# Kernel optimization log

Measured on AMD Instinct MI355X. Metric: run time of the kernel, lower is better.

The kernel has to match this reference:

```python
import jax, jax.numpy as jnp
import numpy as np

EMBED_DIM = 1024
N_HEADS = 16
HEAD_DIM = EMBED_DIM // N_HEADS
B, S = 2, 2048


def setup_inputs() -> dict:
    key = jax.random.key(0)
    ks = jax.random.split(key, 8)
    scale = 1.0 / np.sqrt(EMBED_DIM)
    return {
        "key": jax.random.normal(ks[0], (B, S, EMBED_DIM), jnp.float32),
        "query": jax.random.normal(ks[1], (B, S, EMBED_DIM), jnp.float32),
        "value": jax.random.normal(ks[2], (B, S, EMBED_DIM), jnp.float32),
        # nn.Linear weights stored [out_features, in_features], applied as x @ W.T
        "Wq": jax.random.normal(ks[3], (EMBED_DIM, EMBED_DIM), jnp.float32) * scale,
        "Wk": jax.random.normal(ks[4], (EMBED_DIM, EMBED_DIM), jnp.float32) * scale,
        "Wv": jax.random.normal(ks[5], (EMBED_DIM, EMBED_DIM), jnp.float32) * scale,
        "Wo": jax.random.normal(ks[6], (EMBED_DIM, EMBED_DIM), jnp.float32) * scale,
        "bo": jax.random.normal(ks[7], (EMBED_DIM,), jnp.float32) * scale,
    }


def reference(key, query, value, Wq, Wk, Wv, Wo, bo) -> jnp.ndarray:
    b = key.shape[0]
    # project and split heads: [B, S, E] -> [B, H, S, D]
    def split_heads(x):
        return x.reshape(b, -1, N_HEADS, HEAD_DIM).transpose(0, 2, 1, 3)
    q = split_heads(query @ Wq.T)
    k = split_heads(key @ Wk.T)
    v = split_heads(value @ Wv.T)
    scores = jnp.einsum("bhqd,bhkd->bhqk", q, k) / np.sqrt(HEAD_DIM)
    attn = jax.nn.softmax(scores, axis=-1)
    ctx = jnp.einsum("bhqk,bhkd->bhqd", attn, v)  # [B, H, S, D]
    ctx = ctx.transpose(0, 2, 1, 3).reshape(b, -1, EMBED_DIM)
    return ctx @ Wo.T + bo
```

## Files before the change

### kernel.cpp

```cpp
#include <hip/hip_runtime.h>

typedef unsigned short u16;
typedef __bf16 bf8 __attribute__((ext_vector_type(8)));
typedef __bf16 bf2 __attribute__((ext_vector_type(2)));
typedef float f4 __attribute__((ext_vector_type(4)));

typedef __attribute__((address_space(1))) const unsigned int gas_u32;
typedef __attribute__((address_space(3))) unsigned int las_u32;
#define ASYNC16(g, l) __builtin_amdgcn_global_load_lds((gas_u32*)(g), (las_u32*)(l), 16, 0, 0)

__device__ __forceinline__ u16 f2bf(float f) {
    union { float f; unsigned int u; } v; v.f = f;
    return (u16)((v.u + 0x7fffu + ((v.u >> 16) & 1u)) >> 16);
}

__device__ __forceinline__ unsigned pkbf(float lo, float hi) {
    union { bf2 v; unsigned u; } t;
    t.v[0] = (__bf16)lo;
    t.v[1] = (__bf16)hi;
    return t.u;
}

__device__ __forceinline__ float fexp2(float x) {
#if __has_builtin(__builtin_amdgcn_exp2f)
  return __builtin_amdgcn_exp2f(x);
#else
  return __expf(x * 0.69314718056f);
#endif
}

__global__ __launch_bounds__(256) void cvt_all(
    const float* __restrict__ k_, const float* __restrict__ q_, const float* __restrict__ v_,
    const float* __restrict__ wq, const float* __restrict__ wk, const float* __restrict__ wv,
    const float* __restrict__ wo, u16* __restrict__ ws) {
  size_t e = ((size_t)blockIdx.x * 256 + threadIdx.x) * 8;
  const float* src;
  if      (e <  4194304) src = k_ + e;
  else if (e <  8388608) src = q_ + (e - 4194304);
  else if (e < 12582912) src = v_ + (e - 8388608);
  else if (e < 13631488) src = wq + (e - 12582912);
  else if (e < 14680064) src = wk + (e - 13631488);
  else if (e < 15728640) src = wv + (e - 14680064);
  else                   src = wo + (e - 15728640);
  float4 f0 = ((const float4*)src)[0];
  float4 f1 = ((const float4*)src)[1];
  uint4 o;
  o.x = (unsigned)f2bf(f0.x) | ((unsigned)f2bf(f0.y) << 16);
  o.y = (unsigned)f2bf(f0.z) | ((unsigned)f2bf(f0.w) << 16);
  o.z = (unsigned)f2bf(f1.x) | ((unsigned)f2bf(f1.y) << 16);
  o.w = (unsigned)f2bf(f1.z) | ((unsigned)f2bf(f1.w) << 16);
  *(uint4*)(ws + e) = o;
}

template<int BM, bool FINAL>
__device__ __forceinline__ void gemm_tile(const u16* __restrict__ A, const u16* __restrict__ Bm,
                                          u16* __restrict__ Cb, float* __restrict__ Cf,
                                          const float* __restrict__ bias, float scale,
                                          int bm, int bn, int ldc) {
  __shared__ u16 As[BM*64];
  __shared__ u16 Bs[128*64];
  const int tid = threadIdx.x;
  const int wave = tid >> 6, lane = tid & 63;
  const int wm = wave >> 1, wn = wave & 1;
  const int quad = lane >> 4, l16 = lane & 15;
  const int MI = BM / 32;

  f4 acc[MI][4];
  const f4 zz = {0.f, 0.f, 0.f, 0.f};
  #pragma unroll
  for (int i = 0; i < MI; i++)
    #pragma unroll
    for (int j = 0; j < 4; j++) acc[i][j] = zz;

  const int kr = tid >> 3;
  const int cs = (tid & 7) ^ (kr & 7);
  const u16* ga = A  + (size_t)(bm*BM  + kr)*1024 + cs*8;
  const u16* gb = Bm + (size_t)(bn*128 + kr)*1024 + cs*8;
  u16* la = As + tid*8;
  u16* lb = Bs + tid*8;

  for (int kt = 0; kt < 1024; kt += 64) {
    #pragma unroll
    for (int p = 0; p < BM/32; p++) ASYNC16(ga + (size_t)(p*32)*1024 + kt, la + p*2048);
    #pragma unroll
    for (int p = 0; p < 4; p++)     ASYNC16(gb + (size_t)(p*32)*1024 + kt, lb + p*2048);
    __syncthreads();
    #pragma unroll
    for (int kk = 0; kk < 2; kk++) {
      bf8 af[MI];
      #pragma unroll
      for (int mi = 0; mi < MI; mi++)
        af[mi] = *(const bf8*)(As + (wm*(BM/2) + mi*16 + l16)*64 + (((kk*4 + quad) ^ (l16 & 7))*8));
      #pragma unroll
      for (int ni = 0; ni < 4; ni++) {
        bf8 bfr = *(const bf8*)(Bs + (wn*64 + ni*16 + l16)*64 + (((kk*4 + quad) ^ (l16 & 7))*8));
        #pragma unroll
        for (int mi = 0; mi < MI; mi++)
          acc[mi][ni] = __builtin_amdgcn_mfma_f32_16x16x32_bf16(af[mi], bfr, acc[mi][ni], 0, 0, 0);
      }
    }
    __syncthreads();
  }

  #pragma unroll
  for (int mi = 0; mi < MI; mi++)
    #pragma unroll
    for (int ni = 0; ni < 4; ni++) {
      const int col = bn*128 + wn*64 + ni*16 + l16;
      #pragma unroll
      for (int r = 0; r < 4; r++) {
        const int row = bm*BM + wm*(BM/2) + mi*16 + quad*4 + r;
        if (FINAL) Cf[(size_t)row*ldc + col] = acc[mi][ni][r] + bias[col];
        else       Cb[(size_t)row*ldc + col] = f2bf(acc[mi][ni][r] * scale);
      }
    }
}

#define QSCALE 0.180336880f

__global__ __launch_bounds__(256, 3) void gemm_qkv(
    const u16* __restrict__ xq, const u16* __restrict__ xk, const u16* __restrict__ xv,
    const u16* __restrict__ wq, const u16* __restrict__ wk, const u16* __restrict__ wv,
    u16* __restrict__ Qo, u16* __restrict__ Ko, u16* __restrict__ Vto) {
  if (blockIdx.z == 0)
    gemm_tile<128,false>(xq, wq, Qo, nullptr, nullptr, QSCALE, blockIdx.x, blockIdx.y, 1024);
  else if (blockIdx.z == 1)
    gemm_tile<128,false>(xk, wk, Ko, nullptr, nullptr, 1.0f, blockIdx.x, blockIdx.y, 1024);
  else
    gemm_tile<128,false>(wv, xv, Vto, nullptr, nullptr, 1.0f, blockIdx.y, blockIdx.x, 4096);
}

__global__ __launch_bounds__(256, 2) void gemm_out(
    const u16* __restrict__ ctx, const u16* __restrict__ wo,
    const float* __restrict__ bias, float* __restrict__ out) {
  gemm_tile<64,true>(ctx, wo, nullptr, out, bias, 1.0f, blockIdx.x, blockIdx.y, 1024);
}

__global__ __launch_bounds__(256, 4) void flash_attn(
    const u16* __restrict__ Qg, const u16* __restrict__ Kg,
    const u16* __restrict__ Vtg, u16* __restrict__ ctx) {
  __shared__ uint4 smem4[2208];
  u16* Ks = (u16*)smem4;
  u16* Vt = (u16*)smem4 + 8192;
  float* Of = (float*)smem4;
  float* Lf = (float*)smem4 + 2*64*68;

  const int tid = threadIdx.x;
  const int wave = tid >> 6, lane = tid & 63;
  const int quad = lane >> 4, l16 = lane & 15;
  const int wq = wave >> 1, wk = wave & 1;
  const int h = blockIdx.x, qt = blockIdx.y, b = blockIdx.z;

  bf8 qf[2][2];
  {
    const u16* qp = Qg + (size_t)(b*2048 + qt*64 + wq*32)*1024 + h*64;
    #pragma unroll
    for (int qs = 0; qs < 2; qs++)
      #pragma unroll
      for (int kc = 0; kc < 2; kc++)
        qf[qs][kc] = *(const bf8*)(qp + (size_t)(qs*16 + l16)*1024 + kc*32 + quad*8);
  }

  const f4 zz = {0.f, 0.f, 0.f, 0.f};
  f4 ot[4][2];
  float lrow[2] = {0.f, 0.f};
  #pragma unroll
  for (int ds = 0; ds < 4; ds++)
    #pragma unroll
    for (int qs = 0; qs < 2; qs++) ot[ds][qs] = zz;

  const int kr = tid >> 3;
  const u16* kga = Kg + (size_t)(b*2048 + kr)*1024 + h*64 + ((tid & 7) ^ (kr & 7))*8;
  const int vd = tid >> 4;
  const u16* vga = Vtg + (size_t)(h*64 + vd)*4096 + b*2048 + (((tid & 15) ^ vd))*8;
  u16* kld = Ks + tid*8;
  u16* vld = Vt + tid*8;

  const int prow0 = ((l16 >> 2) << 3) + (l16 & 3);
  const int prow1 = prow0 + 4;

  for (int kv0 = 0; kv0 < 2048; kv0 += 128) {
    __syncthreads();
    #pragma unroll
    for (int p = 0; p < 4; p++) ASYNC16(kga + (size_t)(kv0 + p*32)*1024, kld + p*2048);
    #pragma unroll
    for (int p = 0; p < 4; p++) ASYNC16(vga + (size_t)(p*16)*4096 + kv0, vld + p*2048);
    __syncthreads();

    #pragma unroll
    for (int kb = 0; kb < 2; kb++) {
      f4 st[2][2];
      #pragma unroll
      for (int f = 0; f < 2; f++)
        #pragma unroll
        for (int qs = 0; qs < 2; qs++) st[f][qs] = zz;
      __builtin_amdgcn_s_setprio(1);
      #pragma unroll
      for (int f = 0; f < 2; f++) {
        const int row = wk*64 + kb*32 + (f ? prow1 : prow0);
        #pragma unroll
        for (int kc = 0; kc < 2; kc++) {
          bf8 kf = *(const bf8*)(Ks + row*64 + (((kc*4 + quad) ^ (row & 7))*8));
          #pragma unroll
          for (int qs = 0; qs < 2; qs++)
            st[f][qs] = __builtin_amdgcn_mfma_f32_16x16x32_bf16(kf, qf[qs][kc], st[f][qs], 0, 0, 0);
        }
      }
      __builtin_amdgcn_s_setprio(0);
      bf8 pf[2];
      #pragma unroll
      for (int qs = 0; qs < 2; qs++) {
        float p0 = fexp2(st[0][qs][0]), p1 = fexp2(st[0][qs][1]);
        float p2 = fexp2(st[0][qs][2]), p3 = fexp2(st[0][qs][3]);
        float p4 = fexp2(st[1][qs][0]), p5 = fexp2(st[1][qs][1]);
        float p6 = fexp2(st[1][qs][2]), p7 = fexp2(st[1][qs][3]);
        lrow[qs] += ((p0 + p1) + (p2 + p3)) + ((p4 + p5) + (p6 + p7));
        union { uint4 u; bf8 v; } pu;
        pu.u.x = pkbf(p0, p1);
        pu.u.y = pkbf(p2, p3);
        pu.u.z = pkbf(p4, p5);
        pu.u.w = pkbf(p6, p7);
        pf[qs] = pu.v;
      }
      __builtin_amdgcn_s_setprio(1);
      #pragma unroll
      for (int ds = 0; ds < 4; ds++) {
        const int d = ds*16 + l16;
        bf8 vf = *(const bf8*)(Vt + d*128 + (((wk*8 + kb*4 + quad) ^ l16)*8));
        #pragma unroll
        for (int qs = 0; qs < 2; qs++)
          ot[ds][qs] = __builtin_amdgcn_mfma_f32_16x16x32_bf16(vf, pf[qs], ot[ds][qs], 0, 0, 0);
      }
      __builtin_amdgcn_s_setprio(0);
    }
  }

  __syncthreads();
  #pragma unroll
  for (int qs = 0; qs < 2; qs++) {
    lrow[qs] += __shfl_xor(lrow[qs], 16);
    lrow[qs] += __shfl_xor(lrow[qs], 32);
  }
  float* Ofw = Of + wk*(64*68);
  #pragma unroll
  for (int ds = 0; ds < 4; ds++)
    #pragma unroll
    for (int qs = 0; qs < 2; qs++)
      #pragma unroll
      for (int r = 0; r < 4; r++)
        Ofw[(wq*32 + qs*16 + l16)*68 + ds*16 + quad*4 + r] = ot[ds][qs][r];
  if (quad == 0) {
    Lf[wk*64 + wq*32 + l16]      = lrow[0];
    Lf[wk*64 + wq*32 + 16 + l16] = lrow[1];
  }
  __syncthreads();
  {
    const int qr = tid >> 2, dp = (tid & 3)*16;
    const float inv = 1.f / (Lf[qr] + Lf[64 + qr]);
    const float* o0 = Of + qr*68 + dp;
    const float* o1 = o0 + 64*68;
    unsigned ow[8];
    #pragma unroll
    for (int i = 0; i < 8; i++)
      ow[i] = pkbf((o0[2*i] + o1[2*i]) * inv, (o0[2*i+1] + o1[2*i+1]) * inv);
    u16* cp = ctx + (size_t)(b*2048 + qt*64 + qr)*1024 + h*64 + dp;
    *(uint4*)cp       = *(uint4*)&ow[0];
    *(uint4*)(cp + 8) = *(uint4*)&ow[4];
  }
}

extern "C" void kernel_launch(void* const* d_in, const int* in_sizes, int n_in,
                              void* d_out, int out_size, void* d_ws, size_t ws_size,
                              hipStream_t stream) {
  const float* key_  = (const float*)d_in[0];
  const float* query = (const float*)d_in[1];
  const float* value = (const float*)d_in[2];
  const float* Wq = (const float*)d_in[3];
  const float* Wk = (const float*)d_in[4];
  const float* Wv = (const float*)d_in[5];
  const float* Wo = (const float*)d_in[6];
  const float* bo = (const float*)d_in[7];
  float* out = (float*)d_out;

  u16* ws  = (u16*)d_ws;
  u16* xkb = ws;
  u16* xqb = ws + 4194304;
  u16* xvb = ws + 8388608;
  u16* Wqb = ws + 12582912;
  u16* Wkb = ws + 13631488;
  u16* Wvb = ws + 14680064;
  u16* Wob = ws + 15728640;
  u16* Qb  = ws + 16777216;
  u16* Kb  = ws + 20971520;
  u16* Vtb = ws + 25165824;
  u16* Cb  = ws + 29360128;

  cvt_all<<<8192, 256, 0, stream>>>(key_, query, value, Wq, Wk, Wv, Wo, ws);
  gemm_qkv<<<dim3(32, 8, 3), 256, 0, stream>>>(xqb, xkb, xvb, Wqb, Wkb, Wvb, Qb, Kb, Vtb);
  flash_attn<<<dim3(16, 32, 2), 256, 0, stream>>>(Qb, Kb, Vtb, Cb);
  gemm_out<<<dim3(64, 8), 256, 0, stream>>>(Cb, Wob, bo, out);
}
```

Baseline: 202.7 us.

## Double-buffer K/V tiles in flash attention with async prefetch of next block

```diff
diff --git a/kernel.cpp b/kernel.cpp
--- a/kernel.cpp
+++ b/kernel.cpp
@@ -136,12 +136,11 @@
   gemm_tile<64,true>(ctx, wo, nullptr, out, bias, 1.0f, blockIdx.x, blockIdx.y, 1024);
 }
 
-__global__ __launch_bounds__(256, 4) void flash_attn(
+__global__ __launch_bounds__(256, 2) void flash_attn(
     const u16* __restrict__ Qg, const u16* __restrict__ Kg,
     const u16* __restrict__ Vtg, u16* __restrict__ ctx) {
-  __shared__ uint4 smem4[2208];
-  u16* Ks = (u16*)smem4;
-  u16* Vt = (u16*)smem4 + 8192;
+  __shared__ uint4 smem4[4096];
+  u16* S = (u16*)smem4;
   float* Of = (float*)smem4;
   float* Lf = (float*)smem4 + 2*64*68;
 
@@ -173,19 +172,31 @@
   const u16* kga = Kg + (size_t)(b*2048 + kr)*1024 + h*64 + ((tid & 7) ^ (kr & 7))*8;
   const int vd = tid >> 4;
   const u16* vga = Vtg + (size_t)(h*64 + vd)*4096 + b*2048 + (((tid & 15) ^ vd))*8;
-  u16* kld = Ks + tid*8;
-  u16* vld = Vt + tid*8;
 
   const int prow0 = ((l16 >> 2) << 3) + (l16 & 3);
   const int prow1 = prow0 + 4;
 
-  for (int kv0 = 0; kv0 < 2048; kv0 += 128) {
-    __syncthreads();
-    #pragma unroll
-    for (int p = 0; p < 4; p++) ASYNC16(kga + (size_t)(kv0 + p*32)*1024, kld + p*2048);
-    #pragma unroll
-    for (int p = 0; p < 4; p++) ASYNC16(vga + (size_t)(p*16)*4096 + kv0, vld + p*2048);
-    __syncthreads();
+  #pragma unroll
+  for (int p = 0; p < 4; p++) ASYNC16(kga + (size_t)(p*32)*1024, S + tid*8 + p*2048);
+  #pragma unroll
+  for (int p = 0; p < 4; p++) ASYNC16(vga + (size_t)(p*16)*4096, S + 8192 + tid*8 + p*2048);
+
+  for (int t = 0; t < 16; t++) {
+    u16* Ks = S + (t & 1)*16384;
+    u16* Vt = Ks + 8192;
+    if (t < 15) {
+      u16* kd = S + ((t+1) & 1)*16384 + tid*8;
+      const int kv1 = (t+1)*128;
+      #pragma unroll
+      for (int p = 0; p < 4; p++) ASYNC16(kga + (size_t)(kv1 + p*32)*1024, kd + p*2048);
+      #pragma unroll
+      for (int p = 0; p < 4; p++) ASYNC16(vga + (size_t)(p*16)*4096 + kv1, kd + 8192 + p*2048);
+      asm volatile("s_waitcnt vmcnt(8)" ::: "memory");
+    } else {
+      asm volatile("s_waitcnt vmcnt(0)" ::: "memory");
+    }
+    __builtin_amdgcn_sched_barrier(0);
+    __builtin_amdgcn_s_barrier();
 
     #pragma unroll
     for (int kb = 0; kb < 2; kb++) {
@@ -233,6 +244,9 @@
       }
       __builtin_amdgcn_s_setprio(0);
     }
+
+    asm volatile("s_waitcnt lgkmcnt(0)" ::: "memory");
+    __builtin_amdgcn_s_barrier();
   }
 
   __syncthreads();
```

Result: slower. 211.5 us (+4.4%).

## Overlap next K/V tile async loads with current QK and PV compute

Applied to the files above, without the earlier changes.

```diff
diff --git a/kernel.cpp b/kernel.cpp
--- a/kernel.cpp
+++ b/kernel.cpp
@@ -179,14 +179,16 @@
   const int prow0 = ((l16 >> 2) << 3) + (l16 & 3);
   const int prow1 = prow0 + 4;
 
-  for (int kv0 = 0; kv0 < 2048; kv0 += 128) {
-    __syncthreads();
-    #pragma unroll
-    for (int p = 0; p < 4; p++) ASYNC16(kga + (size_t)(kv0 + p*32)*1024, kld + p*2048);
-    #pragma unroll
-    for (int p = 0; p < 4; p++) ASYNC16(vga + (size_t)(p*16)*4096 + kv0, vld + p*2048);
-    __syncthreads();
-
+  #pragma unroll
+  for (int p = 0; p < 4; p++) ASYNC16(kga + (size_t)(p*32)*1024, kld + p*2048);
+  #pragma unroll
+  for (int p = 0; p < 4; p++) ASYNC16(vga + (size_t)(p*16)*4096, vld + p*2048);
+  asm volatile("s_waitcnt vmcnt(4)" ::: "memory");
+  __builtin_amdgcn_sched_barrier(0);
+  __builtin_amdgcn_s_barrier();
+
+  for (int t = 0; t < 16; t++) {
+    bf8 pf[2][2];
     #pragma unroll
     for (int kb = 0; kb < 2; kb++) {
       f4 st[2][2];
@@ -207,7 +209,6 @@
         }
       }
       __builtin_amdgcn_s_setprio(0);
-      bf8 pf[2];
       #pragma unroll
       for (int qs = 0; qs < 2; qs++) {
         float p0 = fexp2(st[0][qs][0]), p1 = fexp2(st[0][qs][1]);
@@ -220,18 +221,39 @@
         pu.u.y = pkbf(p2, p3);
         pu.u.z = pkbf(p4, p5);
         pu.u.w = pkbf(p6, p7);
-        pf[qs] = pu.v;
-      }
-      __builtin_amdgcn_s_setprio(1);
+        pf[kb][qs] = pu.v;
+      }
+    }
+    asm volatile("s_waitcnt vmcnt(0) lgkmcnt(0)" ::: "memory");
+    __builtin_amdgcn_sched_barrier(0);
+    __builtin_amdgcn_s_barrier();
+    if (t < 15) {
+      const int kv1 = (t + 1) * 128;
+      #pragma unroll
+      for (int p = 0; p < 4; p++) ASYNC16(kga + (size_t)(kv1 + p*32)*1024, kld + p*2048);
+    }
+    __builtin_amdgcn_s_setprio(1);
+    #pragma unroll
+    for (int kb = 0; kb < 2; kb++)
       #pragma unroll
       for (int ds = 0; ds < 4; ds++) {
         const int d = ds*16 + l16;
         bf8 vf = *(const bf8*)(Vt + d*128 + (((wk*8 + kb*4 + quad) ^ l16)*8));
         #pragma unroll
         for (int qs = 0; qs < 2; qs++)
-          ot[ds][qs] = __builtin_amdgcn_mfma_f32_16x16x32_bf16(vf, pf[qs], ot[ds][qs], 0, 0, 0);
-      }
-      __builtin_amdgcn_s_setprio(0);
+          ot[ds][qs] = __builtin_amdgcn_mfma_f32_16x16x32_bf16(vf, pf[kb][qs], ot[ds][qs], 0, 0, 0);
+      }
+    __builtin_amdgcn_s_setprio(0);
+    if (t < 15) {
+      asm volatile("s_waitcnt lgkmcnt(0)" ::: "memory");
+      __builtin_amdgcn_sched_barrier(0);
+      __builtin_amdgcn_s_barrier();
+      const int kv1 = (t + 1) * 128;
+      #pragma unroll
+      for (int p = 0; p < 4; p++) ASYNC16(vga + (size_t)(p*16)*4096 + kv1, vld + p*2048);
+      asm volatile("s_waitcnt vmcnt(4)" ::: "memory");
+      __builtin_amdgcn_sched_barrier(0);
+      __builtin_amdgcn_s_barrier();
     }
   }
 
```

Result: faster. 193.9 us (-4.4%).
